# Kernel optimization log

Measured on AMD Instinct MI355X. Metric: run time of the kernel, lower is better.

Reference implementation:

```python
import jax, jax.numpy as jnp
import numpy as np

HEAD_NUM = 16
QKV_DIM = 16
EMB = 256
MS_HID = 16
B, R, C = 4, 512, 512


def setup_inputs() -> dict:
    key = jax.random.key(0)
    ks = jax.random.split(key, 10)
    inv = 1.0 / np.sqrt(EMB)
    m1 = np.sqrt(0.5)
    m2 = np.sqrt(1.0 / 16.0)
    return {
        "row_emb": jax.random.normal(ks[0], (B, R, EMB), jnp.float32),
        "col_emb": jax.random.normal(ks[1], (B, C, EMB), jnp.float32),
        "cost_mat": jax.random.uniform(ks[2], (B, R, C), jnp.float32),
        # Linear(no bias) weights stored as [in, out] so y = x @ W
        "Wq": jax.random.uniform(ks[3], (EMB, HEAD_NUM * QKV_DIM), jnp.float32, -inv, inv),
        "Wk": jax.random.uniform(ks[4], (EMB, HEAD_NUM * QKV_DIM), jnp.float32, -inv, inv),
        "Wv": jax.random.uniform(ks[5], (EMB, HEAD_NUM * QKV_DIM), jnp.float32, -inv, inv),
        "mix1_weight": jax.random.uniform(ks[6], (HEAD_NUM, 2, MS_HID), jnp.float32, -m1, m1),
        "mix1_bias": jax.random.uniform(ks[7], (HEAD_NUM, MS_HID), jnp.float32, -m1, m1),
        "mix2_weight": jax.random.uniform(ks[8], (HEAD_NUM, MS_HID, 1), jnp.float32, -m2, m2),
        "mix2_bias": jax.random.uniform(ks[9], (HEAD_NUM, 1), jnp.float32, -m2, m2),
    }


def _split_heads(x):
    # [b, g, h*s] -> [b, h, g, s]
    b, g, _ = x.shape
    return x.reshape(b, g, HEAD_NUM, QKV_DIM).transpose(0, 2, 1, 3)


def reference(row_emb, col_emb, cost_mat, Wq, Wk, Wv, mix1_weight, mix1_bias, mix2_weight, mix2_bias):
    q = _split_heads(row_emb @ Wq)  # [b,h,r,s]
    k = _split_heads(col_emb @ Wk)  # [b,h,c,s]
    v = _split_heads(col_emb @ Wv)  # [b,h,c,s]

    dot = jnp.einsum("bhrs,bhcs->bhrc", q, k) / jnp.sqrt(jnp.float32(QKV_DIM))
    cost = jnp.broadcast_to(cost_mat[:, None, :, :], dot.shape)
    two = jnp.stack((dot, cost), axis=-1)  # [b,h,r,c,2]

    # per-head 2-layer MLP applied to each (row, col) score pair
    ms1 = jnp.einsum("bhrcx,hxm->bhrcm", two, mix1_weight) + mix1_bias[None, :, None, None, :]
    ms1 = jax.nn.relu(ms1)
    mixed = jnp.einsum("bhrcm,hmo->bhrco", ms1, mix2_weight)[..., 0] + mix2_bias[None, :, None, None, 0]

    weights = jax.nn.softmax(mixed, axis=3)  # [b,h,r,c]
    out = jnp.einsum("bhrc,bhcs->bhrs", weights, v)
    b, h, r, s = out.shape
    return out.transpose(0, 2, 1, 3).reshape(b, r, h * s)
```

## Files before the change

### kernel.cpp

```cpp
#include <hip/hip_runtime.h>

#define NB 4
#define NH 16
#define RR 512
#define CC 512
#define EMB 256
#define SD 16
#define MH 16

typedef __attribute__((ext_vector_type(4))) float f32x4;
typedef __fp16 half2v __attribute__((ext_vector_type(2)));
typedef __fp16 half4v __attribute__((ext_vector_type(4)));
typedef __fp16 half8v __attribute__((ext_vector_type(8)));

union H8 { half8v v; half2v h[4]; __fp16 e[8]; };
union H4 { half4v v; half2v h[2]; __fp16 e[4]; };

__device__ __forceinline__ unsigned pk_fma(unsigned a, unsigned b, unsigned c) {
  unsigned d;
  asm("v_pk_fma_f16 %0, %1, %2, %3" : "=v"(d) : "v"(a), "v"(b), "v"(c));
  return d;
}
__device__ __forceinline__ unsigned pk_max(unsigned a, unsigned b) {
  unsigned d;
  asm("v_pk_max_f16 %0, %1, %2" : "=v"(d) : "v"(a), "v"(b));
  return d;
}
__device__ __forceinline__ half2v bch(unsigned u) { return __builtin_bit_cast(half2v, u); }
__device__ __forceinline__ unsigned bcu(half2v h) { return __builtin_bit_cast(unsigned, h); }

__global__ __launch_bounds__(256) void prep_w(
    const float* __restrict__ Wq, const float* __restrict__ Wk,
    const float* __restrict__ Wv, __fp16* __restrict__ WT) {
  int bi = blockIdx.x;
  int mat = bi >> 6, chunk = bi & 63;
  const float* src = (mat == 0) ? Wq : (mat == 1) ? Wk : Wv;
  __fp16* dst = WT + mat * (EMB * EMB);
  int t = threadIdx.x;
  int n = chunk * 4 + (t >> 6);
  int e0 = (t & 63) * 4;
  H4 v;
#pragma unroll
  for (int j = 0; j < 4; ++j) v.e[j] = (__fp16)src[(e0 + j) * EMB + n];
  *(half4v*)(dst + n * EMB + e0) = v.v;
}

__global__ __launch_bounds__(256) void proj_kernel(
    const float* __restrict__ rowe, const float* __restrict__ cole,
    const __fp16* __restrict__ WT,
    __fp16* __restrict__ Q, __fp16* __restrict__ K,
    __fp16* __restrict__ VT) {
  int tid = threadIdx.x;
  int wid = tid >> 6, lane = tid & 63, l15 = lane & 15, quad = lane >> 4;
  int wt = blockIdx.x * 4 + wid;
  int mat = wt >> 9;
  int t = wt & 511;
  int rt = t >> 2, ng = t & 3;
  const float* X = (mat == 0) ? rowe : cole;
  const __fp16* Wm = WT + mat * (EMB * EMB);
  const float* xrow = X + (size_t)(rt * 16 + l15) * EMB + quad * 8;

  half8v xf[8];
#pragma unroll
  for (int e = 0; e < 8; ++e) {
    f32x4 b0 = *(const f32x4*)(xrow + e * 32);
    f32x4 b1 = *(const f32x4*)(xrow + e * 32 + 4);
    H8 x;
    x.h[0] = __builtin_amdgcn_cvt_pkrtz(b0[0], b0[1]);
    x.h[1] = __builtin_amdgcn_cvt_pkrtz(b0[2], b0[3]);
    x.h[2] = __builtin_amdgcn_cvt_pkrtz(b1[0], b1[1]);
    x.h[3] = __builtin_amdgcn_cvt_pkrtz(b1[2], b1[3]);
    xf[e] = x.v;
  }
  int row = rt * 16 + l15;
  int b = row >> 9, loc = row & 511;
#pragma unroll
  for (int hh = 0; hh < 4; ++hh) {
    int nt = ng * 4 + hh;
    const half8v* ap = (const half8v*)(Wm + (nt * 16 + l15) * EMB + quad * 8);
    f32x4 acc = {0.f, 0.f, 0.f, 0.f};
#pragma unroll
    for (int e = 0; e < 8; ++e)
      acc = __builtin_amdgcn_mfma_f32_16x16x32_f16(ap[e * 4], xf[e], acc, 0, 0, 0);
    if (mat < 2) {
      H4 pk;
      pk.h[0] = __builtin_amdgcn_cvt_pkrtz(acc[0], acc[1]);
      pk.h[1] = __builtin_amdgcn_cvt_pkrtz(acc[2], acc[3]);
      __fp16* dst = ((mat == 0) ? Q : K) +
          ((size_t)((b * NH + nt) * 512 + loc) * SD + quad * 4);
      *(half4v*)dst = pk.v;
    } else {
#pragma unroll
      for (int i = 0; i < 4; ++i)
        VT[(size_t)((b * NH + nt) * SD + quad * 4 + i) * CC + loc] = (__fp16)acc[i];
    }
  }
}

__global__ __launch_bounds__(256, 4) void attn_kernel(
    const __fp16* __restrict__ Q, const __fp16* __restrict__ K,
    const __fp16* __restrict__ VT, const float* __restrict__ cost,
    const float* __restrict__ m1w, const float* __restrict__ m1b,
    const float* __restrict__ m2w, const float* __restrict__ m2b,
    float* __restrict__ out) {
  __shared__ alignas(16) __fp16 Psh[4][16 * 128];
  __shared__ float Osh[3][256];
  __shared__ float Lsh[4][16];
  int tid = threadIdx.x;
  int wid = tid >> 6, lane = tid & 63, l15 = lane & 15, quad = lane >> 4;
  int rb = blockIdx.x, h = blockIdx.y, b = blockIdx.z;
  int bh = b * NH + h;
  int r0 = rb * 16;
  int cbase = wid * 128;

  unsigned wa2[8], wc2[8], wd2[8], we2[8];
#pragma unroll
  for (int mp = 0; mp < 8; ++mp) {
    wa2[mp] = bcu(half2v{(__fp16)(m1w[(h * 2 + 0) * MH + 2 * mp] * 0.25f),
                         (__fp16)(m1w[(h * 2 + 0) * MH + 2 * mp + 1] * 0.25f)});
    wc2[mp] = bcu(half2v{(__fp16)m1w[(h * 2 + 1) * MH + 2 * mp],
                         (__fp16)m1w[(h * 2 + 1) * MH + 2 * mp + 1]});
    wd2[mp] = bcu(half2v{(__fp16)m1b[h * MH + 2 * mp],
                         (__fp16)m1b[h * MH + 2 * mp + 1]});
    we2[mp] = bcu(half2v{(__fp16)m2w[h * MH + 2 * mp],
                         (__fp16)m2w[h * MH + 2 * mp + 1]});
  }
  float wb2 = m2b[h];
  const half2v one2 = {(__fp16)1.f, (__fp16)1.f};

  half8v qf = {0, 0, 0, 0, 0, 0, 0, 0};
  const __fp16* Qb = Q + (size_t)bh * RR * SD;
  if (quad < 2) qf = *(const half8v*)(Qb + (r0 + l15) * SD + quad * 8);

  const __fp16* Kb = K + ((size_t)bh * CC + cbase) * SD;
  const float* crow = cost + ((size_t)b * RR + r0 + l15) * CC + cbase;
  __fp16* psrow = &Psh[wid][l15 * 128];

  const float L2E = 1.44269504088896f;
  float lsum = 0.f;
  half8v kf_c = *(const half8v*)(Kb + l15 * SD + quad * 8);
  f32x4 cf_c = *(const f32x4*)(crow + quad * 4);
#pragma unroll 4
  for (int it = 0; it < 8; ++it) {
    int itn = (it + 1) & 7;
    half8v kf_n = *(const half8v*)(Kb + (itn * 16 + l15) * SD + quad * 8);
    f32x4 cf_n = *(const f32x4*)(crow + itn * 16 + quad * 4);

    f32x4 acc = {0.f, 0.f, 0.f, 0.f};
    acc = __builtin_amdgcn_mfma_f32_16x16x32_f16(kf_c, qf, acc, 0, 0, 0);
    int c0 = it * 16 + quad * 4;
    float pv[4];
#pragma unroll
    for (int i = 0; i < 4; ++i) {
      unsigned x2 = bcu(__builtin_amdgcn_cvt_pkrtz(acc[i], acc[i]));
      unsigned c2 = bcu(__builtin_amdgcn_cvt_pkrtz(cf_c[i], cf_c[i]));
      float s = wb2;
#pragma unroll
      for (int mp = 0; mp < 8; ++mp) {
        unsigned t1 = pk_fma(wc2[mp], c2, wd2[mp]);
        t1 = pk_fma(wa2[mp], x2, t1);
        t1 = pk_max(t1, 0u);
        s = __builtin_amdgcn_fdot2(bch(we2[mp]), bch(t1), s, false);
      }
      pv[i] = __builtin_amdgcn_exp2f(fmaf(s, L2E, -6.f));
    }
    H4 pk;
    pk.h[0] = __builtin_amdgcn_cvt_pkrtz(pv[0], pv[1]);
    pk.h[1] = __builtin_amdgcn_cvt_pkrtz(pv[2], pv[3]);
    lsum = __builtin_amdgcn_fdot2(pk.h[0], one2, lsum, false);
    lsum = __builtin_amdgcn_fdot2(pk.h[1], one2, lsum, false);
    int g = ((c0 >> 3) ^ (l15 & 7));
    *(half4v*)(psrow + g * 8 + (c0 & 7)) = pk.v;
    kf_c = kf_n; cf_c = cf_n;
  }
  lsum += __shfl_xor(lsum, 16);
  lsum += __shfl_xor(lsum, 32);

  const __fp16* vb = VT + ((size_t)bh * SD + l15) * CC + cbase;
  f32x4 o = {0.f, 0.f, 0.f, 0.f};
  half8v vf_c = *(const half8v*)(vb + quad * 8);
  int g0 = ((quad * 8) >> 3) ^ (l15 & 7);
  H8 pr_c; pr_c.v = *(const half8v*)(psrow + g0 * 8);
#pragma unroll
  for (int it = 0; it < 4; ++it) {
    int itn = (it + 1) & 3;
    half8v vf_n = *(const half8v*)(vb + itn * 32 + quad * 8);
    int c0n = itn * 32 + quad * 8;
    int gn = ((c0n >> 3) ^ (l15 & 7));
    H8 pr_n; pr_n.v = *(const half8v*)(psrow + gn * 8);
    o = __builtin_amdgcn_mfma_f32_16x16x32_f16(pr_c.v, vf_c, o, 0, 0, 0);
    vf_c = vf_n; pr_c = pr_n;
  }

  if (quad == 0) Lsh[wid][l15] = lsum;
  if (wid != 0) {
#pragma unroll
    for (int i = 0; i < 4; ++i) Osh[wid - 1][(quad * 4 + i) * 16 + l15] = o[i];
  }
  __syncthreads();
  if (wid == 0) {
#pragma unroll
    for (int i = 0; i < 4; ++i) {
      int r = quad * 4 + i;
      float l = Lsh[0][r] + Lsh[1][r] + Lsh[2][r] + Lsh[3][r];
      float num = o[i] + Osh[0][r * 16 + l15] + Osh[1][r * 16 + l15] +
                  Osh[2][r * 16 + l15];
      out[((size_t)b * RR + r0 + r) * (NH * SD) + h * SD + l15] = num / l;
    }
  }
}

extern "C" void kernel_launch(void* const* d_in, const int* in_sizes, int n_in,
                              void* d_out, int out_size, void* d_ws, size_t ws_size,
                              hipStream_t stream) {
  const float* rowe = (const float*)d_in[0];
  const float* cole = (const float*)d_in[1];
  const float* cost = (const float*)d_in[2];
  const float* Wq   = (const float*)d_in[3];
  const float* Wk   = (const float*)d_in[4];
  const float* Wv   = (const float*)d_in[5];
  const float* m1w  = (const float*)d_in[6];
  const float* m1b  = (const float*)d_in[7];
  const float* m2w  = (const float*)d_in[8];
  const float* m2b  = (const float*)d_in[9];
  float* outp = (float*)d_out;

  __fp16* ws = (__fp16*)d_ws;
  __fp16* Qw  = ws;
  __fp16* Kw  = ws + 524288;
  __fp16* VTw = ws + 1048576;
  __fp16* WTw = ws + 1572864;

  prep_w<<<dim3(192, 1, 1), 256, 0, stream>>>(Wq, Wk, Wv, WTw);
  proj_kernel<<<dim3(384, 1, 1), 256, 0, stream>>>(rowe, cole, WTw, Qw, Kw, VTw);
  attn_kernel<<<dim3(32, NH, NB), 256, 0, stream>>>(Qw, Kw, VTw, cost,
                                                    m1w, m1b, m2w, m2b, outp);
}
```

Baseline: 116.2 us.

## Feed softmax probabilities directly into PV MFMA from registers, skipping LDS staging

Instead of writing the exponentiated scores to shared memory and reading them back for a second 16x16x32 MFMA loop, each iteration now feeds the packed probabilities straight from registers into a 16x16x16 MFMA with a per-iteration V load. This relies on the QK accumulator layout matching the A-operand layout of the smaller MFMA. All eight cost tiles are also preloaded up front and K is prefetched two iterations ahead. It removes LDS traffic and shared-memory footprint but raises register pressure and uses twice as many smaller MFMAs.

```diff
diff --git a/kernel.cpp b/kernel.cpp
--- a/kernel.cpp
+++ b/kernel.cpp
@@ -103,7 +103,6 @@
     const float* __restrict__ m1w, const float* __restrict__ m1b,
     const float* __restrict__ m2w, const float* __restrict__ m2b,
     float* __restrict__ out) {
-  __shared__ alignas(16) __fp16 Psh[4][16 * 128];
   __shared__ float Osh[3][256];
   __shared__ float Lsh[4][16];
   int tid = threadIdx.x;
@@ -134,26 +133,31 @@
 
   const __fp16* Kb = K + ((size_t)bh * CC + cbase) * SD;
   const float* crow = cost + ((size_t)b * RR + r0 + l15) * CC + cbase;
-  __fp16* psrow = &Psh[wid][l15 * 128];
+  const __fp16* vrow = VT + ((size_t)bh * SD + l15) * CC + cbase;
+
+  f32x4 cf[8];
+#pragma unroll
+  for (int it = 0; it < 8; ++it)
+    cf[it] = *(const f32x4*)(crow + it * 16 + quad * 4);
 
   const float L2E = 1.44269504088896f;
   float lsum = 0.f;
-  half8v kf_c = *(const half8v*)(Kb + l15 * SD + quad * 8);
-  f32x4 cf_c = *(const f32x4*)(crow + quad * 4);
-#pragma unroll 4
+  f32x4 o = {0.f, 0.f, 0.f, 0.f};
+  half8v kf0 = *(const half8v*)(Kb + l15 * SD + quad * 8);
+  half8v kf1 = *(const half8v*)(Kb + (16 + l15) * SD + quad * 8);
+#pragma unroll
   for (int it = 0; it < 8; ++it) {
-    int itn = (it + 1) & 7;
+    int itn = (it + 2) & 7;
     half8v kf_n = *(const half8v*)(Kb + (itn * 16 + l15) * SD + quad * 8);
-    f32x4 cf_n = *(const f32x4*)(crow + itn * 16 + quad * 4);
+    half4v vf = *(const half4v*)(vrow + it * 16 + quad * 4);
 
     f32x4 acc = {0.f, 0.f, 0.f, 0.f};
-    acc = __builtin_amdgcn_mfma_f32_16x16x32_f16(kf_c, qf, acc, 0, 0, 0);
-    int c0 = it * 16 + quad * 4;
+    acc = __builtin_amdgcn_mfma_f32_16x16x32_f16(kf0, qf, acc, 0, 0, 0);
     float pv[4];
 #pragma unroll
     for (int i = 0; i < 4; ++i) {
       unsigned x2 = bcu(__builtin_amdgcn_cvt_pkrtz(acc[i], acc[i]));
-      unsigned c2 = bcu(__builtin_amdgcn_cvt_pkrtz(cf_c[i], cf_c[i]));
+      unsigned c2 = bcu(__builtin_amdgcn_cvt_pkrtz(cf[it][i], cf[it][i]));
       float s = wb2;
 #pragma unroll
       for (int mp = 0; mp < 8; ++mp) {
@@ -169,28 +173,11 @@
     pk.h[1] = __builtin_amdgcn_cvt_pkrtz(pv[2], pv[3]);
     lsum = __builtin_amdgcn_fdot2(pk.h[0], one2, lsum, false);
     lsum = __builtin_amdgcn_fdot2(pk.h[1], one2, lsum, false);
-    int g = ((c0 >> 3) ^ (l15 & 7));
-    *(half4v*)(psrow + g * 8 + (c0 & 7)) = pk.v;
-    kf_c = kf_n; cf_c = cf_n;
+    o = __builtin_amdgcn_mfma_f32_16x16x16f16(pk.v, vf, o, 0, 0, 0);
+    kf0 = kf1; kf1 = kf_n;
   }
   lsum += __shfl_xor(lsum, 16);
   lsum += __shfl_xor(lsum, 32);
-
-  const __fp16* vb = VT + ((size_t)bh * SD + l15) * CC + cbase;
-  f32x4 o = {0.f, 0.f, 0.f, 0.f};
-  half8v vf_c = *(const half8v*)(vb + quad * 8);
-  int g0 = ((quad * 8) >> 3) ^ (l15 & 7);
-  H8 pr_c; pr_c.v = *(const half8v*)(psrow + g0 * 8);
-#pragma unroll
-  for (int it = 0; it < 4; ++it) {
-    int itn = (it + 1) & 3;
-    half8v vf_n = *(const half8v*)(vb + itn * 32 + quad * 8);
-    int c0n = itn * 32 + quad * 8;
-    int gn = ((c0n >> 3) ^ (l15 & 7));
-    H8 pr_n; pr_n.v = *(const half8v*)(psrow + gn * 8);
-    o = __builtin_amdgcn_mfma_f32_16x16x32_f16(pr_c.v, vf_c, o, 0, 0, 0);
-    vf_c = vf_n; pr_c = pr_n;
-  }
 
   if (quad == 0) Lsh[wid][l15] = lsum;
   if (wid != 0) {
```

Measured after the change: 117.3 us. About the same (+0.9%).
